# Optimization experiments

Measured on AMD Instinct MI355X. Metric: run time of the kernel, lower is better.

The kernel has to match this reference:

```python
import jax, jax.numpy as jnp
import numpy as np

N_HEAD = 12
D_HEAD = 64  # inner_dim 768 / 12 heads

def quick_gelu(x):
    return x * jax.nn.sigmoid(1.702 * x)

def setup_inputs() -> dict:
    key = jax.random.key(0)
    ks = jax.random.split(key, 12)
    B, Nv, Lt, Cv, Ct, Ci = 256, 196, 32, 768, 512, 768
    s = lambda k, shp, fan: jax.random.normal(k, shp, jnp.float32) / np.sqrt(fan)
    return {
        "vis_tokens": jax.random.normal(ks[0], (B, Nv, Cv), jnp.float32),
        "text_tokens": jax.random.normal(ks[1], (B, Lt, Ct), jnp.float32),
        "Wq": s(ks[2], (Cv, Ci), Cv), "bq": jnp.zeros((Ci,), jnp.float32),
        "Wk": s(ks[3], (Ct, Ci), Ct), "bk": jnp.zeros((Ci,), jnp.float32),
        "Wv": s(ks[4], (Ct, Ci), Ct), "bv": jnp.zeros((Ci,), jnp.float32),
        "W1": s(ks[5], (Ci, Ci), Ci), "b1": jnp.zeros((Ci,), jnp.float32),
        "W2": s(ks[6], (Ci, 2), Ci), "b2": jnp.zeros((2,), jnp.float32),
    }

def reference(vis_tokens, text_tokens, Wq, bq, Wk, bk, Wv, bv, W1, b1, W2, b2):
    B, Nv, _ = vis_tokens.shape
    Lt = text_tokens.shape[1]
    Ci = Wq.shape[1]
    # projections -> [B, H, N, D]
    q = (vis_tokens @ Wq + bq).reshape(B, Nv, N_HEAD, D_HEAD).transpose(0, 2, 1, 3)
    k = (text_tokens @ Wk + bk).reshape(B, Lt, N_HEAD, D_HEAD).transpose(0, 2, 1, 3)
    v = (text_tokens @ Wv + bv).reshape(B, Lt, N_HEAD, D_HEAD).transpose(0, 2, 1, 3)
    scores = jnp.einsum('bhnd,bhld->bhnl', q, k) / np.sqrt(D_HEAD).astype(np.float32)
    attn = jax.nn.softmax(scores, axis=-1)           # [B,H,Nv,Lt]
    ctx = jnp.einsum('bhnl,bhld->bhnd', attn, v)      # [B,H,Nv,D]
    ctx = ctx.transpose(0, 2, 1, 3).reshape(B, Nv, Ci)
    fused = ctx + vis_tokens[..., :Ci]
    logits = quick_gelu(fused @ W1 + b1) @ W2 + b2    # [B,Nv,2]
    rel_BN = attn.mean(axis=-1).mean(axis=1)          # [B,Nv]
    return (logits, rel_BN)
```

## Files before the change

### kernel.cpp

```cpp
#include <hip/hip_runtime.h>
#include <hip/hip_bf16.h>


typedef __attribute__((ext_vector_type(8))) short bf16x8;
typedef __attribute__((ext_vector_type(4))) float f32x4;

__device__ __forceinline__ float bf2f(unsigned short u) {
    return __uint_as_float(((unsigned int)u) << 16);
}
__device__ __forceinline__ unsigned short f2bf(float f) {
    unsigned int x = __float_as_uint(f);
    unsigned int r = (x + 0x7FFFu + ((x >> 16) & 1u)) >> 16;
    return (unsigned short)r;
}

#define GLOAD_LDS16(gp, lp)                                                    \
    __builtin_amdgcn_global_load_lds(                                          \
        (__attribute__((address_space(1))) void*)(gp),                         \
        (__attribute__((address_space(3))) void*)(lp), 16, 0, 0)

__global__ void cvt_bf16_kernel(const float* __restrict__ in,
                                unsigned short* __restrict__ out, int n4) {
    int i = blockIdx.x * 256 + threadIdx.x;
    if (i >= n4) return;
    float4 v = ((const float4*)in)[i];
    ushort4 o;
    o.x = f2bf(v.x); o.y = f2bf(v.y); o.z = f2bf(v.z); o.w = f2bf(v.w);
    ((ushort4*)out)[i] = o;
}

__global__ void transpose_cvt_kernel(const float* __restrict__ W,
                                     unsigned short* __restrict__ Wt,
                                     int K, int N) {
    __shared__ float tile[32][33];
    int n0 = blockIdx.x * 32, k0 = blockIdx.y * 32;
    int tx = threadIdx.x & 31, ty = threadIdx.x >> 5;
    #pragma unroll
    for (int r = ty; r < 32; r += 8)
        tile[r][tx] = W[(size_t)(k0 + r) * N + n0 + tx];
    __syncthreads();
    #pragma unroll
    for (int r = ty; r < 32; r += 8)
        Wt[(size_t)(n0 + r) * K + k0 + tx] = f2bf(tile[tx][r]);
}

template<int KTOT, int GELU, int MTILES>
__global__ __launch_bounds__(256, 2)
void gemm_bt_kernel(const unsigned short* __restrict__ A,
                    const unsigned short* __restrict__ Bt,
                    const float* __restrict__ bias,
                    unsigned short* __restrict__ C) {
    constexpr int GS = 520;
    __shared__ unsigned short As[16 * GS];
    __shared__ unsigned short Bs[16 * GS];
    const int tid = threadIdx.x;
    const int lane = tid & 63, wave = tid >> 6;
    const int id = blockIdx.x;
    const int xcd = id & 7, local = id >> 3;
    const int nt = local % 6, mt = xcd * (MTILES / 8) + local / 6;
    const size_t m0 = (size_t)mt * 128;
    const int n0 = nt * 128;
    const int wm = (wave >> 1) * 64, wn = (wave & 1) * 64;
    const int lr = lane & 15, quad = lane >> 4;

    const int swz = ((lane & 7) ^ (lane >> 3)) * 8;
    const unsigned short* gA = A + (m0 + wave * 32 + (lane >> 3)) * KTOT + swz;
    const unsigned short* gB = Bt + ((size_t)n0 + wave * 32 + (lane >> 3)) * KTOT + swz;
    unsigned short* lA = As + (wave * 4) * GS;
    unsigned short* lB = Bs + (wave * 4) * GS;

    f32x4 acc[4][4] = {};

    for (int kt = 0; kt < KTOT; kt += 64) {
        #pragma unroll
        for (int i = 0; i < 4; ++i) {
            GLOAD_LDS16(gA + (size_t)i * 8 * KTOT + kt, lA + i * GS);
            GLOAD_LDS16(gB + (size_t)i * 8 * KTOT + kt, lB + i * GS);
        }
        __syncthreads();
        #pragma unroll
        for (int kk = 0; kk < 64; kk += 32) {
            bf16x8 fa[4], fb[4];
            #pragma unroll
            for (int i = 0; i < 4; ++i) {
                int r = wm + i * 16 + lr;
                int g = (kk >> 3) + quad;
                fa[i] = *(const bf16x8*)(As + (r >> 3) * GS + (r & 7) * 64 +
                                         ((g ^ (r & 7)) << 3));
            }
            #pragma unroll
            for (int j = 0; j < 4; ++j) {
                int r = wn + j * 16 + lr;
                int g = (kk >> 3) + quad;
                fb[j] = *(const bf16x8*)(Bs + (r >> 3) * GS + (r & 7) * 64 +
                                         ((g ^ (r & 7)) << 3));
            }
            #pragma unroll
            for (int i = 0; i < 4; ++i)
                #pragma unroll
                for (int j = 0; j < 4; ++j)
                    acc[i][j] = __builtin_amdgcn_mfma_f32_16x16x32_bf16(
                        fa[i], fb[j], acc[i][j], 0, 0, 0);
        }
        __syncthreads();
    }

    #pragma unroll
    for (int j = 0; j < 4; ++j) {
        int col = n0 + wn + j * 16 + lr;
        float bv = bias[col];
        #pragma unroll
        for (int i = 0; i < 4; ++i) {
            #pragma unroll
            for (int r = 0; r < 4; ++r) {
                size_t row = m0 + wm + i * 16 + quad * 4 + r;
                float x = acc[i][j][r] + bv;
                if (GELU) x = x / (1.0f + __expf(-1.702f * x));
                C[row * 768 + col] = f2bf(x);
            }
        }
    }
}

__global__ __launch_bounds__(256, 4)
void attn_mfma_kernel(const unsigned short* __restrict__ Q,
                      const unsigned short* __restrict__ Kb,
                      const unsigned short* __restrict__ Vb,
                      unsigned short* __restrict__ RF) {
    constexpr int KS = 72;
    constexpr int VS = 34;
    constexpr int PS = 40;
    constexpr int CS = 72;
    __shared__ unsigned short Ks[32 * KS];
    __shared__ unsigned short Vt[64 * VS];
    __shared__ unsigned short Pb[4][16 * PS];
    __shared__ unsigned short Cb[4][16 * CS];
    const int tid = threadIdx.x;
    const int b = blockIdx.x / 12, h = blockIdx.x % 12;
    const int lane = tid & 63, wave = tid >> 6;
    const int lr = lane & 15, quad = lane >> 4;

    {
        int l = tid >> 3, d8 = (tid & 7) * 8;
        size_t base = ((size_t)b * 32 + l) * 768 + (size_t)h * 64 + d8;
        bf16x8 kv = *(const bf16x8*)(Kb + base);
        bf16x8 vv = *(const bf16x8*)(Vb + base);
        *(bf16x8*)(Ks + l * KS + d8) = kv;
        #pragma unroll
        for (int j = 0; j < 8; ++j)
            Vt[(d8 + j) * VS + l] = (unsigned short)vv[j];
    }
    __syncthreads();

    bf16x8 fbK[2][2];
    #pragma unroll
    for (int n = 0; n < 2; ++n)
        #pragma unroll
        for (int ks = 0; ks < 2; ++ks)
            fbK[n][ks] = *(const bf16x8*)(Ks + (n * 16 + lr) * KS + ks * 32 + quad * 8);
    bf16x8 fbV[4];
    #pragma unroll
    for (int d = 0; d < 4; ++d)
        fbV[d] = *(const bf16x8*)(Vt + (d * 16 + lr) * VS + quad * 8);

    const size_t qbase = (size_t)b * 196 * 768 + (size_t)h * 64;

    for (int t = wave; t < 13; t += 4) {
        const int m0 = t * 16;
        int qrow = m0 + lr; if (qrow > 195) qrow = 195;
        const unsigned short* qp = Q + qbase + (size_t)qrow * 768;
        bf16x8 fa0 = *(const bf16x8*)(qp + quad * 8);
        bf16x8 fa1 = *(const bf16x8*)(qp + 32 + quad * 8);
        f32x4 s0 = {}, s1 = {};
        s0 = __builtin_amdgcn_mfma_f32_16x16x32_bf16(fa0, fbK[0][0], s0, 0, 0, 0);
        s0 = __builtin_amdgcn_mfma_f32_16x16x32_bf16(fa1, fbK[0][1], s0, 0, 0, 0);
        s1 = __builtin_amdgcn_mfma_f32_16x16x32_bf16(fa0, fbK[1][0], s1, 0, 0, 0);
        s1 = __builtin_amdgcn_mfma_f32_16x16x32_bf16(fa1, fbK[1][1], s1, 0, 0, 0);

        float p0[4], p1[4], m4[4], s4[4];
        #pragma unroll
        for (int r = 0; r < 4; ++r) {
            p0[r] = s0[r] * 0.125f;
            p1[r] = s1[r] * 0.125f;
            m4[r] = fmaxf(p0[r], p1[r]);
        }
        #pragma unroll
        for (int off = 1; off < 16; off <<= 1)
            #pragma unroll
            for (int r = 0; r < 4; ++r)
                m4[r] = fmaxf(m4[r], __shfl_xor(m4[r], off));
        #pragma unroll
        for (int r = 0; r < 4; ++r) {
            p0[r] = __expf(p0[r] - m4[r]);
            p1[r] = __expf(p1[r] - m4[r]);
            s4[r] = p0[r] + p1[r];
        }
        #pragma unroll
        for (int off = 1; off < 16; off <<= 1)
            #pragma unroll
            for (int r = 0; r < 4; ++r)
                s4[r] += __shfl_xor(s4[r], off);
        #pragma unroll
        for (int r = 0; r < 4; ++r) {
            float inv = __builtin_amdgcn_rcpf(s4[r]);
            unsigned short* pr = &Pb[wave][(quad * 4 + r) * PS];
            pr[lr]      = f2bf(p0[r] * inv);
            pr[16 + lr] = f2bf(p1[r] * inv);
        }

        bf16x8 fap = *(const bf16x8*)(&Pb[wave][lr * PS + quad * 8]);
        f32x4 c[4];
        #pragma unroll
        for (int d = 0; d < 4; ++d) {
            f32x4 z = {};
            c[d] = __builtin_amdgcn_mfma_f32_16x16x32_bf16(fap, fbV[d], z, 0, 0, 0);
        }
        #pragma unroll
        for (int d = 0; d < 4; ++d)
            #pragma unroll
            for (int r = 0; r < 4; ++r)
                Cb[wave][(quad * 4 + r) * CS + d * 16 + lr] = f2bf(c[d][r]);
        #pragma unroll
        for (int i = 0; i < 2; ++i) {
            int c2 = lane + i * 64;
            int row = c2 >> 3, col8 = (c2 & 7) * 8;
            int grow = m0 + row;
            if (grow < 196) {
                bf16x8 cv = *(const bf16x8*)(&Cb[wave][row * CS + col8]);
                unsigned short* gp = RF + qbase + (size_t)grow * 768 + col8;
                bf16x8 rv = *(const bf16x8*)gp;
                bf16x8 ov;
                #pragma unroll
                for (int j = 0; j < 8; ++j)
                    ov[j] = (short)f2bf(bf2f((unsigned short)cv[j]) +
                                        bf2f((unsigned short)rv[j]));
                *(bf16x8*)gp = ov;
            }
        }
    }
}

__global__ __launch_bounds__(256)
void mlp2_kernel(const unsigned short* __restrict__ Hb,
                 const float* __restrict__ W2,
                 const float* __restrict__ b2,
                 float* __restrict__ out) {
    __shared__ float w2s[2][768];
    const int tid = threadIdx.x;
    for (int i = tid; i < 1536; i += 256) w2s[i & 1][i >> 1] = W2[i];
    __syncthreads();
    const int sub = tid & 7;
    const int r = tid >> 3;
    const size_t row = (size_t)blockIdx.x * 32 + r;
    float a0 = 0.f, a1 = 0.f;
    #pragma unroll
    for (int i = 0; i < 12; ++i) {
        int base = i * 64 + sub * 8;
        bf16x8 hv = *(const bf16x8*)(Hb + row * 768 + base);
        #pragma unroll
        for (int j = 0; j < 8; ++j) {
            float hf = bf2f((unsigned short)hv[j]);
            a0 += hf * w2s[0][base + j];
            a1 += hf * w2s[1][base + j];
        }
    }
    #pragma unroll
    for (int o = 4; o >= 1; o >>= 1) {
        a0 += __shfl_down(a0, o, 8);
        a1 += __shfl_down(a1, o, 8);
    }
    if (sub == 0) {
        out[row * 2]      = a0 + b2[0];
        out[row * 2 + 1]  = a1 + b2[1];
        out[100352 + row] = 0.03125f;
    }
}

extern "C" void kernel_launch(void* const* d_in, const int* in_sizes, int n_in,
                              void* d_out, int out_size, void* d_ws, size_t ws_size,
                              hipStream_t stream) {
    const float* vis = (const float*)d_in[0];
    const float* txt = (const float*)d_in[1];
    const float* Wq  = (const float*)d_in[2];
    const float* bq  = (const float*)d_in[3];
    const float* Wk  = (const float*)d_in[4];
    const float* bk  = (const float*)d_in[5];
    const float* Wv  = (const float*)d_in[6];
    const float* bv  = (const float*)d_in[7];
    const float* W1  = (const float*)d_in[8];
    const float* b1  = (const float*)d_in[9];
    const float* W2  = (const float*)d_in[10];
    const float* b2  = (const float*)d_in[11];
    float* out = (float*)d_out;

    char* w = (char*)d_ws;
    unsigned short* Abf = (unsigned short*)(w);
    unsigned short* Tbf = (unsigned short*)(w + 77070336);
    unsigned short* Wqt = (unsigned short*)(w + 85458944);
    unsigned short* Wkt = (unsigned short*)(w + 86638592);
    unsigned short* Wvt = (unsigned short*)(w + 87425024);
    unsigned short* W1t = (unsigned short*)(w + 88211456);
    unsigned short* Qbf = (unsigned short*)(w + 89391104);
    unsigned short* Kbf = (unsigned short*)(w + 166461440);
    unsigned short* Vbf = (unsigned short*)(w + 179044352);
    unsigned short* Hbf = Qbf;

    cvt_bf16_kernel<<<37632, 256, 0, stream>>>(vis, Abf, 9633792);
    cvt_bf16_kernel<<<4096, 256, 0, stream>>>(txt, Tbf, 1048576);
    transpose_cvt_kernel<<<dim3(24, 24), 256, 0, stream>>>(Wq, Wqt, 768, 768);
    transpose_cvt_kernel<<<dim3(24, 16), 256, 0, stream>>>(Wk, Wkt, 512, 768);
    transpose_cvt_kernel<<<dim3(24, 16), 256, 0, stream>>>(Wv, Wvt, 512, 768);
    transpose_cvt_kernel<<<dim3(24, 24), 256, 0, stream>>>(W1, W1t, 768, 768);

    gemm_bt_kernel<768, 0, 392><<<2352, 256, 0, stream>>>(Abf, Wqt, bq, Qbf);
    gemm_bt_kernel<512, 0, 64><<<384, 256, 0, stream>>>(Tbf, Wkt, bk, Kbf);
    gemm_bt_kernel<512, 0, 64><<<384, 256, 0, stream>>>(Tbf, Wvt, bv, Vbf);

    attn_mfma_kernel<<<3072, 256, 0, stream>>>(Qbf, Kbf, Vbf, Abf);

    gemm_bt_kernel<768, 1, 392><<<2352, 256, 0, stream>>>(Abf, W1t, b1, Hbf);

    mlp2_kernel<<<1568, 256, 0, stream>>>(Hbf, W2, b2, out);
}
```

Measured before the change: 495.1 us.

## Use 256x256-tile 8-wave GEMM with interleaved LDS prefetch for Q and W1 projections

Adds a new bf16 MFMA GEMM that gives each 512-thread workgroup a 256x256 output tile, double-buffers K-tiles of 64 in LDS, and interleaves global-to-LDS loads with four MFMA quarter-phases under explicit waitcnt and barrier control and raised wave priority. The two large GEMMs (the Q projection and the W1 layer with GELU) switch from the 128x128 kernel to this one. Larger tiles raise arithmetic intensity and cut redundant global loads, and the finer scheduling aims to hide load latency. The cost is one workgroup per CU with a heavy register footprint, and only 588 workgroups to spread across the CUs.

```diff
diff --git a/kernel.cpp b/kernel.cpp
--- a/kernel.cpp
+++ b/kernel.cpp
@@ -18,6 +18,12 @@
     __builtin_amdgcn_global_load_lds(                                          \
         (__attribute__((address_space(1))) void*)(gp),                         \
         (__attribute__((address_space(3))) void*)(lp), 16, 0, 0)
+
+#define BAR()  __builtin_amdgcn_s_barrier()
+#define LGKM0 asm volatile("s_waitcnt lgkmcnt(0)" ::: "memory")
+#define VMC0  asm volatile("s_waitcnt vmcnt(0)" ::: "memory")
+#define VMC4  asm volatile("s_waitcnt vmcnt(4)" ::: "memory")
+#define VMC6  asm volatile("s_waitcnt vmcnt(6)" ::: "memory")
 
 __global__ void cvt_bf16_kernel(const float* __restrict__ in,
                                 unsigned short* __restrict__ out, int n4) {
@@ -42,6 +48,146 @@
     #pragma unroll
     for (int r = ty; r < 32; r += 8)
         Wt[(size_t)(n0 + r) * K + k0 + tx] = f2bf(tile[tx][r]);
+}
+
+template<int KTOT, int GELU>
+__global__ __launch_bounds__(512, 1)
+void gemm256_kernel(const unsigned short* __restrict__ A,
+                    const unsigned short* __restrict__ Bt,
+                    const float* __restrict__ bias,
+                    unsigned short* __restrict__ C) {
+    constexpr int NT = KTOT / 64;
+    constexpr int GS = 520;
+    constexpr int TSZ = 32 * GS;
+    __shared__ unsigned short As[2 * TSZ];
+    __shared__ unsigned short Bs[2 * TSZ];
+    const int tid = threadIdx.x;
+    const int lane = tid & 63, wave = tid >> 6;
+    const int wm = wave >> 2, wn = wave & 3;
+    const int lr = lane & 15, quad = lane >> 4;
+    const int s7 = lane & 7;
+    const int rp = ((lr >> 3) * GS) + ((lane & 7) << 6);
+
+    const int nwg = gridDim.x;
+    const int qq = nwg >> 3, r8 = nwg & 7;
+    const int xcd = blockIdx.x & 7, loc = blockIdx.x >> 3;
+    const int wg = (xcd < r8 ? xcd * (qq + 1) : r8 * (qq + 1) + (xcd - r8) * qq) + loc;
+    const int mt = wg / 3, nt = wg - mt * 3;
+    const size_t m0 = (size_t)mt * 256;
+    const int n0 = nt * 256;
+
+    const int swz = ((lane & 7) ^ (lane >> 3)) * 8;
+    const unsigned short* gA = A + (m0 + (lane >> 3)) * (size_t)KTOT + swz;
+    const unsigned short* gB = Bt + ((size_t)(n0 + (lane >> 3))) * KTOT + swz;
+
+#define STG_A(b, t, h) do {                                                    \
+    const int g0_ = (h) * 16 + wave * 2;                                       \
+    GLOAD_LDS16(gA + (size_t)(g0_) * 8 * KTOT + (t) * 64,                      \
+                As + (b) * TSZ + (g0_) * GS);                                  \
+    GLOAD_LDS16(gA + (size_t)(g0_ + 1) * 8 * KTOT + (t) * 64,                  \
+                As + (b) * TSZ + (g0_ + 1) * GS);                              \
+} while (0)
+#define STG_B(b, t, h) do {                                                    \
+    const int g0_ = (h) * 16 + wave * 2;                                       \
+    GLOAD_LDS16(gB + (size_t)(g0_) * 8 * KTOT + (t) * 64,                      \
+                Bs + (b) * TSZ + (g0_) * GS);                                  \
+    GLOAD_LDS16(gB + (size_t)(g0_ + 1) * 8 * KTOT + (t) * 64,                  \
+                Bs + (b) * TSZ + (g0_ + 1) * GS);                              \
+} while (0)
+
+    f32x4 acc[8][4] = {};
+    bf16x8 aR[4][2], bR[4][2];
+
+#define LDA_FRAGS(ibase)                                                       \
+    _Pragma("unroll")                                                          \
+    for (int i = 0; i < 4; ++i)                                                \
+        _Pragma("unroll")                                                      \
+        for (int kk = 0; kk < 2; ++kk)                                         \
+            aR[i][kk] = *(const bf16x8*)(pa + (wm * 16 + ((ibase) + i) * 2) * GS \
+                         + rp + ((((kk * 4) + quad) ^ s7) << 3));
+
+#define LDB_FRAGS(jbase)                                                       \
+    _Pragma("unroll")                                                          \
+    for (int j = 0; j < 2; ++j)                                                \
+        _Pragma("unroll")                                                      \
+        for (int kk = 0; kk < 2; ++kk)                                         \
+            bR[(jbase) + j][kk] = *(const bf16x8*)(pb + (wn * 8 + ((jbase) + j) * 2) * GS \
+                         + rp + ((((kk * 4) + quad) ^ s7) << 3));
+
+#define MFMA_Q(I0, J0)                                                         \
+    __builtin_amdgcn_s_setprio(1);                                             \
+    _Pragma("unroll")                                                          \
+    for (int i = 0; i < 4; ++i)                                                \
+        _Pragma("unroll")                                                      \
+        for (int j = 0; j < 2; ++j)                                            \
+            _Pragma("unroll")                                                  \
+            for (int kk = 0; kk < 2; ++kk)                                     \
+                acc[(I0) + i][(J0) + j] = __builtin_amdgcn_mfma_f32_16x16x32_bf16( \
+                    aR[i][kk], bR[(J0) + j][kk], acc[(I0) + i][(J0) + j], 0, 0, 0); \
+    __builtin_amdgcn_s_setprio(0);
+
+    STG_B(0, 0, 0); STG_B(0, 0, 1); STG_A(0, 0, 0); STG_A(0, 0, 1);
+    VMC4;
+    STG_B(1, 1, 0); STG_B(1, 1, 1); STG_A(1, 1, 0);
+    VMC6;
+    BAR();
+
+    for (int t = 0; t < NT - 1; ++t) {
+        const int buf = t & 1;
+        const unsigned short* pa = As + buf * TSZ;
+        const unsigned short* pb = Bs + buf * TSZ;
+        const bool last = (t == NT - 2);
+        LDA_FRAGS(0); LDB_FRAGS(0);
+        STG_A(buf ^ 1, t + 1, 1);
+        BAR(); LGKM0;
+        MFMA_Q(0, 0);
+        BAR();
+        LDB_FRAGS(2);
+        BAR(); LGKM0;
+        MFMA_Q(0, 2);
+        BAR();
+        LDA_FRAGS(4);
+        if (!last) { STG_B(buf, t + 2, 0); } else { VMC4; }
+        BAR(); LGKM0;
+        MFMA_Q(4, 0);
+        BAR();
+        if (!last) { STG_B(buf, t + 2, 1); STG_A(buf, t + 2, 0); VMC6; }
+        else { VMC0; }
+        BAR(); LGKM0;
+        MFMA_Q(4, 2);
+        BAR();
+    }
+    {
+        const unsigned short* pa = As + ((NT - 1) & 1) * TSZ;
+        const unsigned short* pb = Bs + ((NT - 1) & 1) * TSZ;
+        LDA_FRAGS(0); LDB_FRAGS(0); LDB_FRAGS(2);
+        MFMA_Q(0, 0);
+        MFMA_Q(0, 2);
+        LDA_FRAGS(4);
+        MFMA_Q(4, 0);
+        MFMA_Q(4, 2);
+    }
+
+    #pragma unroll
+    for (int j = 0; j < 4; ++j) {
+        int col = n0 + wn * 64 + j * 16 + lr;
+        float bv = bias[col];
+        #pragma unroll
+        for (int i = 0; i < 8; ++i) {
+            #pragma unroll
+            for (int r2 = 0; r2 < 4; ++r2) {
+                size_t row = m0 + wm * 128 + i * 16 + quad * 4 + r2;
+                float x = acc[i][j][r2] + bv;
+                if (GELU) x = x / (1.0f + __expf(-1.702f * x));
+                C[row * 768 + col] = f2bf(x);
+            }
+        }
+    }
+#undef STG_A
+#undef STG_B
+#undef LDA_FRAGS
+#undef LDB_FRAGS
+#undef MFMA_Q
 }
 
 template<int KTOT, int GELU, int MTILES>
@@ -312,13 +458,13 @@
     transpose_cvt_kernel<<<dim3(24, 16), 256, 0, stream>>>(Wv, Wvt, 512, 768);
     transpose_cvt_kernel<<<dim3(24, 24), 256, 0, stream>>>(W1, W1t, 768, 768);
 
-    gemm_bt_kernel<768, 0, 392><<<2352, 256, 0, stream>>>(Abf, Wqt, bq, Qbf);
+    gemm256_kernel<768, 0><<<588, 512, 0, stream>>>(Abf, Wqt, bq, Qbf);
     gemm_bt_kernel<512, 0, 64><<<384, 256, 0, stream>>>(Tbf, Wkt, bk, Kbf);
     gemm_bt_kernel<512, 0, 64><<<384, 256, 0, stream>>>(Tbf, Wvt, bv, Vbf);
 
     attn_mfma_kernel<<<3072, 256, 0, stream>>>(Qbf, Kbf, Vbf, Abf);
 
-    gemm_bt_kernel<768, 1, 392><<<2352, 256, 0, stream>>>(Abf, W1t, b1, Hbf);
+    gemm256_kernel<768, 1><<<588, 512, 0, stream>>>(Abf, W1t, b1, Hbf);
 
     mlp2_kernel<<<1568, 256, 0, stream>>>(Hbf, W2, b2, out);
 }
```

Result: slower. 560.3 us (+13.2%).

## Double-buffer GEMM LDS tiles and merge prep and K/V launches

Applied to the files above, without the earlier changes.

The bf16 GEMM now keeps two LDS stages, each split into two 32-wide K panels with a new XOR swizzle, and prefetches tile t+2 while computing tile t using explicit vmcnt waits and barriers. The goal is to hide global-to-LDS load latency that the old single-buffer loop exposed with a full sync every 64-wide K step. The input conversions, the four weight transposes and the K and V projections are each merged into a single launch to cut launch overhead and idle gaps. LDS use per block doubles to 64KB, which may limit how many blocks fit on a CU, and the hand-placed waitcnt scheduling has to stay correct.

```diff
diff --git a/kernel.cpp b/kernel.cpp
--- a/kernel.cpp
+++ b/kernel.cpp
@@ -19,25 +19,40 @@
         (__attribute__((address_space(1))) void*)(gp),                         \
         (__attribute__((address_space(3))) void*)(lp), 16, 0, 0)
 
-__global__ void cvt_bf16_kernel(const float* __restrict__ in,
-                                unsigned short* __restrict__ out, int n4) {
+#define BAR()  __builtin_amdgcn_s_barrier()
+#define SCHED0 __builtin_amdgcn_sched_barrier(0)
+#define VMC0  asm volatile("s_waitcnt vmcnt(0)" ::: "memory")
+#define VMC8  asm volatile("s_waitcnt vmcnt(8)" ::: "memory")
+
+__global__ void cvt2_kernel(const float* __restrict__ in0,
+                            unsigned short* __restrict__ out0, int n0,
+                            const float* __restrict__ in1,
+                            unsigned short* __restrict__ out1) {
     int i = blockIdx.x * 256 + threadIdx.x;
-    if (i >= n4) return;
+    const float* in = in0; unsigned short* out = out0;
+    if (i >= n0) { i -= n0; in = in1; out = out1; }
     float4 v = ((const float4*)in)[i];
     ushort4 o;
     o.x = f2bf(v.x); o.y = f2bf(v.y); o.z = f2bf(v.z); o.w = f2bf(v.w);
     ((ushort4*)out)[i] = o;
 }
 
-__global__ void transpose_cvt_kernel(const float* __restrict__ W,
-                                     unsigned short* __restrict__ Wt,
-                                     int K, int N) {
+__global__ void transpose4_kernel(const float* __restrict__ Wq, unsigned short* __restrict__ Wqt,
+                                  const float* __restrict__ Wk, unsigned short* __restrict__ Wkt,
+                                  const float* __restrict__ Wv, unsigned short* __restrict__ Wvt,
+                                  const float* __restrict__ W1, unsigned short* __restrict__ W1t) {
     __shared__ float tile[32][33];
-    int n0 = blockIdx.x * 32, k0 = blockIdx.y * 32;
+    int id = blockIdx.x;
+    const float* W; unsigned short* Wt; int K;
+    if (id < 576)       { W = Wq; Wt = Wqt; K = 768; }
+    else if (id < 960)  { id -= 576;  W = Wk; Wt = Wkt; K = 512; }
+    else if (id < 1344) { id -= 960;  W = Wv; Wt = Wvt; K = 512; }
+    else                { id -= 1344; W = W1; Wt = W1t; K = 768; }
+    int n0 = (id % 24) * 32, k0 = (id / 24) * 32;
     int tx = threadIdx.x & 31, ty = threadIdx.x >> 5;
     #pragma unroll
     for (int r = ty; r < 32; r += 8)
-        tile[r][tx] = W[(size_t)(k0 + r) * N + n0 + tx];
+        tile[r][tx] = W[(size_t)(k0 + r) * 768 + n0 + tx];
     __syncthreads();
     #pragma unroll
     for (int r = ty; r < 32; r += 8)
@@ -45,81 +60,134 @@
 }
 
 template<int KTOT, int GELU, int MTILES>
-__global__ __launch_bounds__(256, 2)
-void gemm_bt_kernel(const unsigned short* __restrict__ A,
-                    const unsigned short* __restrict__ Bt,
-                    const float* __restrict__ bias,
-                    unsigned short* __restrict__ C) {
-    constexpr int GS = 520;
-    __shared__ unsigned short As[16 * GS];
-    __shared__ unsigned short Bs[16 * GS];
+__device__ __forceinline__
+void gemm_body(int id, const unsigned short* __restrict__ A,
+               const unsigned short* __restrict__ Bt,
+               const float* __restrict__ bias,
+               unsigned short* __restrict__ C,
+               unsigned short* As, unsigned short* Bs) {
+    constexpr int NT = KTOT / 64;
+    constexpr int PAN = 4096;
+    constexpr int TSZ = 2 * PAN;
     const int tid = threadIdx.x;
     const int lane = tid & 63, wave = tid >> 6;
-    const int id = blockIdx.x;
+    const int wm = (wave >> 1) * 64, wn = (wave & 1) * 64;
+    const int lr = lane & 15, quad = lane >> 4;
+
     const int xcd = id & 7, local = id >> 3;
     const int nt = local % 6, mt = xcd * (MTILES / 8) + local / 6;
     const size_t m0 = (size_t)mt * 128;
     const int n0 = nt * 128;
-    const int wm = (wave >> 1) * 64, wn = (wave & 1) * 64;
-    const int lr = lane & 15, quad = lane >> 4;
-
-    const int swz = ((lane & 7) ^ (lane >> 3)) * 8;
-    const unsigned short* gA = A + (m0 + wave * 32 + (lane >> 3)) * KTOT + swz;
-    const unsigned short* gB = Bt + ((size_t)n0 + wave * 32 + (lane >> 3)) * KTOT + swz;
-    unsigned short* lA = As + (wave * 4) * GS;
-    unsigned short* lB = Bs + (wave * 4) * GS;
+
+    const int slotoff = ((quad ^ (((lr >> 3) & 1) << 1)) << 3);
+    const int aBase = (wm + lr) * 32 + slotoff;
+    const int bBase = (wn + lr) * 32 + slotoff;
+
+    const int sg = (lane & 3) ^ (((lane >> 5) & 1) << 1);
+    const unsigned short* gA = A + (m0 + (lane >> 2)) * (size_t)KTOT + sg * 8;
+    const unsigned short* gB = Bt + ((size_t)n0 + (lane >> 2)) * KTOT + sg * 8;
+    const int sr = wave * 32;
+
+#define STG(b, t) do {                                                         \
+    _Pragma("unroll")                                                          \
+    for (int p_ = 0; p_ < 2; ++p_) {                                           \
+        _Pragma("unroll")                                                      \
+        for (int q_ = 0; q_ < 2; ++q_) {                                       \
+            const int r0_ = sr + q_ * 16;                                      \
+            GLOAD_LDS16(gA + (size_t)r0_ * KTOT + (t) * 64 + p_ * 32,          \
+                        As + (b) * TSZ + p_ * PAN + r0_ * 32);                 \
+            GLOAD_LDS16(gB + (size_t)r0_ * KTOT + (t) * 64 + p_ * 32,          \
+                        Bs + (b) * TSZ + p_ * PAN + r0_ * 32);                 \
+        }                                                                      \
+    }                                                                          \
+} while (0)
 
     f32x4 acc[4][4] = {};
 
-    for (int kt = 0; kt < KTOT; kt += 64) {
-        #pragma unroll
-        for (int i = 0; i < 4; ++i) {
-            GLOAD_LDS16(gA + (size_t)i * 8 * KTOT + kt, lA + i * GS);
-            GLOAD_LDS16(gB + (size_t)i * 8 * KTOT + kt, lB + i * GS);
-        }
-        __syncthreads();
-        #pragma unroll
-        for (int kk = 0; kk < 64; kk += 32) {
-            bf16x8 fa[4], fb[4];
-            #pragma unroll
-            for (int i = 0; i < 4; ++i) {
-                int r = wm + i * 16 + lr;
-                int g = (kk >> 3) + quad;
-                fa[i] = *(const bf16x8*)(As + (r >> 3) * GS + (r & 7) * 64 +
-                                         ((g ^ (r & 7)) << 3));
-            }
+#define COMPUTE(bsel) do {                                                     \
+    const unsigned short* pa = As + (bsel) * TSZ;                              \
+    const unsigned short* pb = Bs + (bsel) * TSZ;                              \
+    _Pragma("unroll")                                                          \
+    for (int kk = 0; kk < 2; ++kk) {                                           \
+        bf16x8 fa[4], fb[4];                                                   \
+        _Pragma("unroll")                                                      \
+        for (int i = 0; i < 4; ++i)                                            \
+            fa[i] = *(const bf16x8*)(pa + kk * PAN + aBase + i * 512);         \
+        _Pragma("unroll")                                                      \
+        for (int j = 0; j < 4; ++j)                                            \
+            fb[j] = *(const bf16x8*)(pb + kk * PAN + bBase + j * 512);         \
+        _Pragma("unroll")                                                      \
+        for (int i = 0; i < 4; ++i)                                            \
+            _Pragma("unroll")                                                  \
+            for (int j = 0; j < 4; ++j)                                        \
+                acc[i][j] = __builtin_amdgcn_mfma_f32_16x16x32_bf16(           \
+                    fa[i], fb[j], acc[i][j], 0, 0, 0);                         \
+    }                                                                          \
+} while (0)
+
+    STG(0, 0);
+    STG(1, 1);
+    VMC8;
+    BAR(); SCHED0;
+
+    for (int t = 0; t < NT - 1; ++t) {
+        COMPUTE(t & 1);
+        BAR(); SCHED0;
+        if (t + 2 < NT) { STG(t & 1, t + 2); VMC8; }
+        else            { VMC0; }
+        BAR(); SCHED0;
+    }
+    COMPUTE((NT - 1) & 1);
+
+    float bvv[4];
+    #pragma unroll
+    for (int j = 0; j < 4; ++j)
+        bvv[j] = bias[n0 + wn + j * 16 + lr];
+    #pragma unroll
+    for (int i = 0; i < 4; ++i) {
+        #pragma unroll
+        for (int r2 = 0; r2 < 4; ++r2) {
+            size_t row = m0 + wm + i * 16 + quad * 4 + r2;
+            unsigned short* cp = C + row * 768 + n0 + wn + lr;
             #pragma unroll
             for (int j = 0; j < 4; ++j) {
-                int r = wn + j * 16 + lr;
-                int g = (kk >> 3) + quad;
-                fb[j] = *(const bf16x8*)(Bs + (r >> 3) * GS + (r & 7) * 64 +
-                                         ((g ^ (r & 7)) << 3));
+                float x = acc[i][j][r2] + bvv[j];
+                if (GELU) x = x / (1.0f + __expf(-1.702f * x));
+                cp[j * 16] = f2bf(x);
             }
-            #pragma unroll
-            for (int i = 0; i < 4; ++i)
-                #pragma unroll
-                for (int j = 0; j < 4; ++j)
-                    acc[i][j] = __builtin_amdgcn_mfma_f32_16x16x32_bf16(
-                        fa[i], fb[j], acc[i][j], 0, 0, 0);
-        }
-        __syncthreads();
-    }
-
-    #pragma unroll
-    for (int j = 0; j < 4; ++j) {
-        int col = n0 + wn + j * 16 + lr;
-        float bv = bias[col];
-        #pragma unroll
-        for (int i = 0; i < 4; ++i) {
-            #pragma unroll
-            for (int r = 0; r < 4; ++r) {
-                size_t row = m0 + wm + i * 16 + quad * 4 + r;
-                float x = acc[i][j][r] + bv;
-                if (GELU) x = x / (1.0f + __expf(-1.702f * x));
-                C[row * 768 + col] = f2bf(x);
-            }
-        }
-    }
+        }
+    }
+#undef STG
+#undef COMPUTE
+}
+
+template<int KTOT, int GELU, int MTILES>
+__global__ __launch_bounds__(256, 2)
+void gemm_db_kernel(const unsigned short* __restrict__ A,
+                    const unsigned short* __restrict__ Bt,
+                    const float* __restrict__ bias,
+                    unsigned short* __restrict__ C) {
+    __shared__ unsigned short As[2 * 8192];
+    __shared__ unsigned short Bs[2 * 8192];
+    gemm_body<KTOT, GELU, MTILES>(blockIdx.x, A, Bt, bias, C, As, Bs);
+}
+
+template<int KTOT, int MTILES>
+__global__ __launch_bounds__(256, 2)
+void gemm_kv_kernel(const unsigned short* __restrict__ A,
+                    const unsigned short* __restrict__ Bt0,
+                    const float* __restrict__ bias0,
+                    unsigned short* __restrict__ C0,
+                    const unsigned short* __restrict__ Bt1,
+                    const float* __restrict__ bias1,
+                    unsigned short* __restrict__ C1) {
+    __shared__ unsigned short As[2 * 8192];
+    __shared__ unsigned short Bs[2 * 8192];
+    const int half = gridDim.x >> 1;
+    if (blockIdx.x < half)
+        gemm_body<KTOT, 0, MTILES>(blockIdx.x, A, Bt0, bias0, C0, As, Bs);
+    else
+        gemm_body<KTOT, 0, MTILES>(blockIdx.x - half, A, Bt1, bias1, C1, As, Bs);
 }
 
 __global__ __launch_bounds__(256, 4)
@@ -305,20 +373,15 @@
     unsigned short* Vbf = (unsigned short*)(w + 179044352);
     unsigned short* Hbf = Qbf;
 
-    cvt_bf16_kernel<<<37632, 256, 0, stream>>>(vis, Abf, 9633792);
-    cvt_bf16_kernel<<<4096, 256, 0, stream>>>(txt, Tbf, 1048576);
-    transpose_cvt_kernel<<<dim3(24, 24), 256, 0, stream>>>(Wq, Wqt, 768, 768);
-    transpose_cvt_kernel<<<dim3(24, 16), 256, 0, stream>>>(Wk, Wkt, 512, 768);
-    transpose_cvt_kernel<<<dim3(24, 16), 256, 0, stream>>>(Wv, Wvt, 512, 768);
-    transpose_cvt_kernel<<<dim3(24, 24), 256, 0, stream>>>(W1, W1t, 768, 768);
-
-    gemm_bt_kernel<768, 0, 392><<<2352, 256, 0, stream>>>(Abf, Wqt, bq, Qbf);
-    gemm_bt_kernel<512, 0, 64><<<384, 256, 0, stream>>>(Tbf, Wkt, bk, Kbf);
-    gemm_bt_kernel<512, 0, 64><<<384, 256, 0, stream>>>(Tbf, Wvt, bv, Vbf);
+    cvt2_kernel<<<41728, 256, 0, stream>>>(vis, Abf, 9633792, txt, Tbf);
+    transpose4_kernel<<<1920, 256, 0, stream>>>(Wq, Wqt, Wk, Wkt, Wv, Wvt, W1, W1t);
+
+    gemm_db_kernel<768, 0, 392><<<2352, 256, 0, stream>>>(Abf, Wqt, bq, Qbf);
+    gemm_kv_kernel<512, 64><<<768, 256, 0, stream>>>(Tbf, Wkt, bk, Kbf, Wvt, bv, Vbf);
 
     attn_mfma_kernel<<<3072, 256, 0, stream>>>(Qbf, Kbf, Vbf, Abf);
 
-    gemm_bt_kernel<768, 1, 392><<<2352, 256, 0, stream>>>(Abf, W1t, b1, Hbf);
+    gemm_db_kernel<768, 1, 392><<<2352, 256, 0, stream>>>(Abf, W1t, b1, Hbf);
 
     mlp2_kernel<<<1568, 256, 0, stream>>>(Hbf, W2, b2, out);
 }
```

Result: slower. 511.2 us (+3.3%).
